# Kernel optimization log

Hardware: AMD Instinct MI355X
Metric: run time of the kernel (lower is better)

The kernel has to match this reference:

```python
import jax, jax.numpy as jnp
import numpy as np

B, T, D = 2, 2048, 1024
H, DK, DV = 16, 64, 64
DFF = 4096
EPS = 1e-6


def layer_norm(x, gamma, beta):
    # Matches the torch module: unbiased std (ddof=1), eps added to std,
    # gamma multiplied before dividing by (std + eps).
    mean = x.mean(axis=-1, keepdims=True)
    std = x.std(axis=-1, ddof=1, keepdims=True)
    return (x - mean) * gamma / (std + EPS) + beta


def setup_inputs() -> dict:
    key = jax.random.key(0)
    ks = jax.random.split(key, 8)
    s = 0.02
    return {
        "x": jax.random.normal(ks[0], (B, T, D), dtype=jnp.float32),
        "w_q": jax.random.normal(ks[1], (D, H * DK), dtype=jnp.float32) * s,
        "w_k": jax.random.normal(ks[2], (D, H * DK), dtype=jnp.float32) * s,
        "w_v": jax.random.normal(ks[3], (D, H * DV), dtype=jnp.float32) * s,
        "w_o": jax.random.normal(ks[4], (H * DV, D), dtype=jnp.float32) * s,
        "b_o": jnp.zeros((D,), dtype=jnp.float32),
        "w_fc1": jax.random.normal(ks[5], (D, DFF), dtype=jnp.float32) * s,
        "b_fc1": jnp.zeros((DFF,), dtype=jnp.float32),
        "w_fc2": jax.random.normal(ks[6], (DFF, D), dtype=jnp.float32) * s,
        "b_fc2": jnp.zeros((D,), dtype=jnp.float32),
        "ln1_g": jnp.ones((D,), dtype=jnp.float32),
        "ln1_b": jnp.zeros((D,), dtype=jnp.float32),
        "ln2_g": jnp.ones((D,), dtype=jnp.float32),
        "ln2_b": jnp.zeros((D,), dtype=jnp.float32),
    }


def attention(h, w_q, w_k, w_v, w_o, b_o):
    b, t, _ = h.shape
    q = (h @ w_q).reshape(b, t, H, DK).transpose(0, 2, 1, 3)  # [b,h,t,dk]
    k = (h @ w_k).reshape(b, t, H, DK).transpose(0, 2, 1, 3)
    v = (h @ w_v).reshape(b, t, H, DV).transpose(0, 2, 1, 3)
    scores = jnp.einsum('bhqk,bhmk->bhqm', q, k)              # [b,h,t,t]
    causal = jnp.triu(jnp.ones((t, t), dtype=bool), k=1)
    scores = jnp.where(causal, -jnp.inf, scores)
    attn = jax.nn.softmax(scores / jnp.sqrt(jnp.float32(DK)), axis=-1)
    ctx = jnp.einsum('bhqm,bhmv->bhqv', attn, v)              # [b,h,t,dv]
    ctx = ctx.transpose(0, 2, 1, 3).reshape(b, t, H * DV)
    return ctx @ w_o + b_o


def reference(x, w_q, w_k, w_v, w_o, b_o, w_fc1, b_fc1, w_fc2, b_fc2,
              ln1_g, ln1_b, ln2_g, ln2_b):
    x = x + attention(layer_norm(x, ln1_g, ln1_b), w_q, w_k, w_v, w_o, b_o)
    h = layer_norm(x, ln2_g, ln2_b)
    mlp = jax.nn.gelu(h @ w_fc1 + b_fc1, approximate=False) @ w_fc2 + b_fc2
    return x + mlp
```

## Files before the change

### kernel.cpp

```cpp
#include <hip/hip_runtime.h>
#include <hip/hip_bf16.h>
#include <cstdint>

#define Bz 2
#define Tz 2048
#define Dz 1024
#define Hz 16
#define NR (Bz*Tz)

typedef __bf16 bf16;
typedef __bf16 bf16x8 __attribute__((ext_vector_type(8)));
typedef __bf16 bf16x4 __attribute__((ext_vector_type(4)));
typedef short  s16x4  __attribute__((ext_vector_type(4)));
typedef float  f32x4  __attribute__((ext_vector_type(4)));

typedef unsigned int u32as1 __attribute__((address_space(1)));
typedef unsigned int u32as3 __attribute__((address_space(3)));

__device__ __forceinline__ void gl2lds16(const void* gp, void* lp) {
    __builtin_amdgcn_global_load_lds((u32as1*)gp, (u32as3*)lp, 16, 0, 0);
}

__global__ void k_transpose_cvt(const float* __restrict__ W, bf16* __restrict__ WT,
                                int K, int N, float scale) {
    __shared__ float tile[32][33];
    const int n0 = blockIdx.x * 32, k0 = blockIdx.y * 32;
    const int tx = threadIdx.x, ty = threadIdx.y;
#pragma unroll
    for (int i = 0; i < 4; i++)
        tile[ty + i*8][tx] = W[(size_t)(k0 + ty + i*8) * N + n0 + tx];
    __syncthreads();
#pragma unroll
    for (int i = 0; i < 4; i++)
        WT[(size_t)(n0 + ty + i*8) * K + k0 + tx] = (bf16)(tile[tx][ty + i*8] * scale);
}

__global__ void k_vtrans(const bf16* __restrict__ qkv, bf16* __restrict__ Vt) {
    __shared__ bf16 tile[64][72];
    const int t0 = blockIdx.x * 64;
    const int bh = blockIdx.y;
    const int b = bh >> 4, h = bh & 15;
    const int tid = threadIdx.x;
    const int tr = tid >> 3, c8 = (tid & 7) * 8;
    const bf16* src = qkv + (size_t)b * Tz * 3072 + 2048 + h * 64;
#pragma unroll
    for (int i = 0; i < 2; i++) {
        bf16x8 v = *(const bf16x8*)(src + (size_t)(t0 + i*32 + tr) * 3072 + c8);
        *(bf16x8*)&tile[i*32 + tr][c8] = v;
    }
    __syncthreads();
    bf16* dst = Vt + (size_t)bh * 64 * Tz + t0;
#pragma unroll
    for (int i = 0; i < 2; i++) {
        const int vr = i*32 + tr;
        bf16x8 o;
#pragma unroll
        for (int j = 0; j < 8; j++) o[j] = tile[c8 + j][vr];
        *(bf16x8*)(dst + (size_t)vr * Tz + c8) = o;
    }
}

__global__ void k_layernorm(const float* __restrict__ X, const float* __restrict__ gam,
                            const float* __restrict__ bet, bf16* __restrict__ out) {
    const int row = blockIdx.x, t = threadIdx.x;
    const float4 v = ((const float4*)(X + (size_t)row * Dz))[t];
    float s  = v.x + v.y + v.z + v.w;
    float ss = v.x*v.x + v.y*v.y + v.z*v.z + v.w*v.w;
#pragma unroll
    for (int o = 1; o < 64; o <<= 1) { s += __shfl_xor(s, o); ss += __shfl_xor(ss, o); }
    __shared__ float rs[4], rss[4];
    if ((t & 63) == 0) { rs[t >> 6] = s; rss[t >> 6] = ss; }
    __syncthreads();
    s  = rs[0] + rs[1] + rs[2] + rs[3];
    ss = rss[0] + rss[1] + rss[2] + rss[3];
    const float mean = s * (1.f / Dz);
    const float var  = fmaxf((ss - s * mean) * (1.f / (Dz - 1)), 0.f);
    const float inv  = 1.f / (sqrtf(var) + 1e-6f);
    const float4 gv = ((const float4*)gam)[t];
    const float4 bv = ((const float4*)bet)[t];
    bf16x4 o;
    o[0] = (bf16)((v.x - mean) * gv.x * inv + bv.x);
    o[1] = (bf16)((v.y - mean) * gv.y * inv + bv.y);
    o[2] = (bf16)((v.z - mean) * gv.z * inv + bv.z);
    o[3] = (bf16)((v.w - mean) * gv.w * inv + bv.w);
    *(bf16x4*)(out + (size_t)row * Dz + t * 4) = o;
}

__global__ __launch_bounds__(256) void k_gemm(
    const bf16* __restrict__ A, const bf16* __restrict__ BT,
    int M, int N, int K,
    const float* __restrict__ bias, const float* __restrict__ resid,
    float* __restrict__ Cf, bf16* __restrict__ Cb, int act,
    float* __restrict__ Cpart, int nsplit)
{
    __shared__ bf16 lA[128 * 64];
    __shared__ bf16 lB[128 * 64];
    const int tid = threadIdx.x;
    const int w = tid >> 6, lane = tid & 63;
    const int q = lane >> 4, l16 = lane & 15;
    const int m0 = blockIdx.y * 128, n0 = blockIdx.x * 128;
    const int wm = (w >> 1) * 64, wn = (w & 1) * 64;

    const int srow = lane >> 3;
    const int skg  = (lane & 7) ^ srow;
    const bf16* Ab = A  + (size_t)(m0 + w * 32 + srow) * K + skg * 8;
    const bf16* Bb = BT + (size_t)(n0 + w * 32 + srow) * K + skg * 8;
    bf16* lAw = lA + w * 2048;
    bf16* lBw = lB + w * 2048;

    f32x4 acc[4][4] = {};

    const int kPer = K / nsplit;
    const int kBeg = blockIdx.z * kPer, kEnd = kBeg + kPer;
    for (int k0 = kBeg; k0 < kEnd; k0 += 64) {
#pragma unroll
        for (int i = 0; i < 4; i++) {
            gl2lds16(Ab + (size_t)i * 8 * K + k0, lAw + i * 512);
            gl2lds16(Bb + (size_t)i * 8 * K + k0, lBw + i * 512);
        }
        __syncthreads();
#pragma unroll
        for (int kh = 0; kh < 2; kh++) {
            const int sl = (((kh * 4 + q) ^ (l16 & 7)) * 8);
            bf16x8 af[4], bfr[4];
#pragma unroll
            for (int t = 0; t < 4; t++) {
                af[t]  = *(const bf16x8*)(lA + (wm + t * 16 + l16) * 64 + sl);
                bfr[t] = *(const bf16x8*)(lB + (wn + t * 16 + l16) * 64 + sl);
            }
#pragma unroll
            for (int i = 0; i < 4; i++)
#pragma unroll
                for (int j = 0; j < 4; j++)
                    acc[i][j] = __builtin_amdgcn_mfma_f32_16x16x32_bf16(
                        af[i], bfr[j], acc[i][j], 0, 0, 0);
        }
        __syncthreads();
    }

    if (nsplit > 1) {
        float* P = Cpart + (size_t)blockIdx.z * M * N;
#pragma unroll
        for (int i = 0; i < 4; i++) {
            const int gr = m0 + wm + i * 16 + q * 4;
#pragma unroll
            for (int j = 0; j < 4; j++) {
                const int gc = n0 + wn + j * 16 + l16;
#pragma unroll
                for (int r = 0; r < 4; r++)
                    P[(size_t)(gr + r) * N + gc] = acc[i][j][r];
            }
        }
        return;
    }

#pragma unroll
    for (int i = 0; i < 4; i++) {
        const int gr = m0 + wm + i * 16 + q * 4;
#pragma unroll
        for (int j = 0; j < 4; j++) {
            const int gc = n0 + wn + j * 16 + l16;
            const float bv = bias ? bias[gc] : 0.f;
#pragma unroll
            for (int r = 0; r < 4; r++) {
                float v = acc[i][j][r] + bv;
                if (act) v = 0.5f * v * (1.f + erff(v * 0.70710678118f));
                const size_t idx = (size_t)(gr + r) * N + gc;
                if (resid) v += resid[idx];
                if (Cf) Cf[idx] = v;
                else    Cb[idx] = (bf16)v;
            }
        }
    }
}

__global__ __launch_bounds__(256) void k_reduce(
    const float* __restrict__ part, int nsplit, size_t MN, int N,
    const float* __restrict__ bias, const float* __restrict__ resid,
    float* __restrict__ Cf, bf16* __restrict__ Cb, int act)
{
    const size_t i4 = ((size_t)blockIdx.x * 256 + threadIdx.x) * 4;
    float4 v = *(const float4*)(part + i4);
    for (int s = 1; s < nsplit; s++) {
        const float4 p = *(const float4*)(part + s * MN + i4);
        v.x += p.x; v.y += p.y; v.z += p.z; v.w += p.w;
    }
    const int col = (int)(i4 % N);
    if (bias) {
        const float4 bv = *(const float4*)(bias + col);
        v.x += bv.x; v.y += bv.y; v.z += bv.z; v.w += bv.w;
    }
    if (act) {
        v.x = 0.5f * v.x * (1.f + erff(v.x * 0.70710678118f));
        v.y = 0.5f * v.y * (1.f + erff(v.y * 0.70710678118f));
        v.z = 0.5f * v.z * (1.f + erff(v.z * 0.70710678118f));
        v.w = 0.5f * v.w * (1.f + erff(v.w * 0.70710678118f));
    }
    if (resid) {
        const float4 rv = *(const float4*)(resid + i4);
        v.x += rv.x; v.y += rv.y; v.z += rv.z; v.w += rv.w;
    }
    if (Cf) *(float4*)(Cf + i4) = v;
    else {
        bf16x4 o; o[0] = (bf16)v.x; o[1] = (bf16)v.y; o[2] = (bf16)v.z; o[3] = (bf16)v.w;
        *(bf16x4*)(Cb + i4) = o;
    }
}

__global__ __launch_bounds__(256) void k_attn(const bf16* __restrict__ qkv,
                                              const bf16* __restrict__ Vt,
                                              bf16* __restrict__ ctx)
{
    __shared__ __align__(16) char smem[34816];
    bf16* lK = (bf16*)smem;
    bf16* lV = (bf16*)(smem + 16384);
    f32x4* sAcc = (f32x4*)smem;
    float*  sM  = (float*)(smem + 32768);
    float*  sL  = (float*)(smem + 33792);

    const int tid = threadIdx.x, lane = tid & 63, w = tid >> 6;
    const int l16 = lane & 15, quad = lane >> 4;
    const int wq = w & 1, ws = w >> 1;
    const int pr = blockIdx.x;
    const int h = blockIdx.y, b = blockIdx.z;

    const bf16* Qp  = qkv + (size_t)b * Tz * 3072 + h * 64;
    const bf16* Kp  = Qp + 1024;
    const bf16* Vtp = Vt + (size_t)(b * Hz + h) * 64 * Tz;

    const int krow  = tid >> 3;
    const int kslot = (tid & 7) ^ (krow & 7);
    const bf16* Kg = Kp + (size_t)krow * 3072 + kslot * 8;
    const int vrow  = tid >> 4;
    const int vslot = (tid & 15) ^ (vrow & 7);
    const bf16* Vg = Vtp + (size_t)vrow * Tz + vslot * 8;

#pragma unroll
    for (int ti = 0; ti < 2; ti++) {
        const int t = ti ? (63 - pr) : pr;
        const int q0 = t * 32 + wq * 16;

        bf16x8 qf[2];
#pragma unroll
        for (int kh = 0; kh < 2; kh++)
            qf[kh] = *(const bf16x8*)(Qp + (size_t)(q0 + l16) * 3072 + kh*32 + quad*8);

        f32x4 acc[4] = {};
        float m = -1e30f, l = 0.f;

        const int keyEnd = t * 32 + 32;
        for (int ktB = 0; ktB < keyEnd; ktB += 128) {
            __syncthreads();
#pragma unroll
            for (int s = 0; s < 4; s++) {
                gl2lds16(Kg + (size_t)(ktB + s * 32) * 3072, lK + s * 2048 + w * 512);
                gl2lds16(Vg + (size_t)s * 16 * Tz + ktB,     lV + s * 2048 + w * 512);
            }
            __syncthreads();

            const int kt = ktB + ws * 64;
            if (kt <= q0 + 15) {
                f32x4 sv[4];
                const int sw = l16 & 7;
#pragma unroll
                for (int c = 0; c < 4; c++) {
                    const int R = ws * 64 + c * 16 + l16;
                    bf16x8 kf0 = *(const bf16x8*)(lK + R * 64 + ((quad     ^ sw) * 8));
                    bf16x8 kf1 = *(const bf16x8*)(lK + R * 64 + (((4+quad) ^ sw) * 8));
                    f32x4 z = {0.f, 0.f, 0.f, 0.f};
                    z = __builtin_amdgcn_mfma_f32_16x16x32_bf16(kf0, qf[0], z, 0, 0, 0);
                    z = __builtin_amdgcn_mfma_f32_16x16x32_bf16(kf1, qf[1], z, 0, 0, 0);
                    sv[c] = z;
                }
                if (kt + 63 > q0) {
#pragma unroll
                    for (int c = 0; c < 4; c++)
#pragma unroll
                        for (int r = 0; r < 4; r++)
                            if (kt + c*16 + quad*4 + r > q0 + l16) sv[c][r] = -1e30f;
                }
                float t0 = fmaxf(fmaxf(sv[0][0], sv[0][1]), fmaxf(sv[0][2], sv[0][3]));
                float t1 = fmaxf(fmaxf(sv[1][0], sv[1][1]), fmaxf(sv[1][2], sv[1][3]));
                float t2 = fmaxf(fmaxf(sv[2][0], sv[2][1]), fmaxf(sv[2][2], sv[2][3]));
                float t3 = fmaxf(fmaxf(sv[3][0], sv[3][1]), fmaxf(sv[3][2], sv[3][3]));
                float tm = fmaxf(fmaxf(t0, t1), fmaxf(t2, t3));
                tm = fmaxf(tm, __shfl_xor(tm, 16));
                tm = fmaxf(tm, __shfl_xor(tm, 32));
                if (__any(tm > m)) {
                    const float mn = fmaxf(m, tm);
                    const float a  = __expf(m - mn);
                    m = mn;
                    l *= a;
#pragma unroll
                    for (int vt = 0; vt < 4; vt++)
#pragma unroll
                        for (int r = 0; r < 4; r++) acc[vt][r] *= a;
                }
                float ts = 0.f;
#pragma unroll
                for (int c = 0; c < 4; c++) {
                    s16x4 vf[4];
                    const int gslot = ws * 8 + c * 2 + (quad >> 1);
#pragma unroll
                    for (int vt = 0; vt < 4; vt++) {
                        const int Rv = vt * 16 + l16;
                        vf[vt] = *(const s16x4*)(lV + Rv * 128 + ((gslot ^ (Rv & 7)) * 8)
                                                 + (quad & 1) * 4);
                    }
                    bf16x4 tb;
#pragma unroll
                    for (int r = 0; r < 4; r++) {
                        const float p = __expf(sv[c][r] - m);
                        ts += p;
                        tb[r] = (bf16)p;
                    }
                    const s16x4 pb = __builtin_bit_cast(s16x4, tb);
#pragma unroll
                    for (int vt = 0; vt < 4; vt++)
                        acc[vt] = __builtin_amdgcn_mfma_f32_16x16x16bf16_1k(
                            vf[vt], pb, acc[vt], 0, 0, 0);
                }
                ts += __shfl_xor(ts, 16);
                ts += __shfl_xor(ts, 32);
                l += ts;
            }
        }

        __syncthreads();
        if (ws == 1) {
            sM[wq * 64 + lane] = m;
            sL[wq * 64 + lane] = l;
#pragma unroll
            for (int vt = 0; vt < 4; vt++)
                sAcc[(wq * 4 + vt) * 64 + lane] = acc[vt];
        }
        __syncthreads();
        if (ws == 0) {
            const float m1 = sM[wq * 64 + lane], l1 = sL[wq * 64 + lane];
            const float M  = fmaxf(m, m1);
            const float a0 = __expf(m - M), a1 = __expf(m1 - M);
            const float inv = 1.f / (l * a0 + l1 * a1);
#pragma unroll
            for (int vt = 0; vt < 4; vt++) {
                const f32x4 o1 = sAcc[(wq * 4 + vt) * 64 + lane];
                bf16x4 o;
#pragma unroll
                for (int r = 0; r < 4; r++)
                    o[r] = (bf16)((acc[vt][r] * a0 + o1[r] * a1) * inv);
                *(bf16x4*)(ctx + (size_t)(b * Tz + q0 + l16) * 1024
                           + h * 64 + vt * 16 + quad * 4) = o;
            }
        }
    }
}

extern "C" void kernel_launch(void* const* d_in, const int* in_sizes, int n_in,
                              void* d_out, int out_size, void* d_ws, size_t ws_size,
                              hipStream_t stream)
{
    const float* x     = (const float*)d_in[0];
    const float* w_q   = (const float*)d_in[1];
    const float* w_k   = (const float*)d_in[2];
    const float* w_v   = (const float*)d_in[3];
    const float* w_o   = (const float*)d_in[4];
    const float* b_o   = (const float*)d_in[5];
    const float* w_fc1 = (const float*)d_in[6];
    const float* b_fc1 = (const float*)d_in[7];
    const float* w_fc2 = (const float*)d_in[8];
    const float* b_fc2 = (const float*)d_in[9];
    const float* ln1_g = (const float*)d_in[10];
    const float* ln1_b = (const float*)d_in[11];
    const float* ln2_g = (const float*)d_in[12];
    const float* ln2_b = (const float*)d_in[13];
    float* out = (float*)d_out;

    char* p = (char*)d_ws;
    bf16* wqkvT = (bf16*)p; p += (size_t)3072 * 1024 * 2;
    bf16* woT   = (bf16*)p; p += (size_t)1024 * 1024 * 2;
    bf16* wfc1T = (bf16*)p; p += (size_t)4096 * 1024 * 2;
    bf16* wfc2T = (bf16*)p; p += (size_t)1024 * 4096 * 2;
    bf16* h1    = (bf16*)p; p += (size_t)NR * 1024 * 2;
    bf16* qkv   = (bf16*)p; p += (size_t)NR * 3072 * 2;
    bf16* ctx   = (bf16*)p; p += (size_t)NR * 1024 * 2;
    float* y    = (float*)p; p += (size_t)NR * 1024 * 4;
    bf16* h2    = (bf16*)p; p += (size_t)NR * 1024 * 2;
    bf16* g     = (bf16*)p; p += (size_t)NR * 4096 * 2;
    bf16* Vt    = h1;
    float* projPart = (float*)g;
    float* fc2Part  = (float*)h1;

    const dim3 tb(32, 8);
    k_transpose_cvt<<<dim3(32, 32),  tb, 0, stream>>>(w_q,   wqkvT,             1024, 1024, 0.125f);
    k_transpose_cvt<<<dim3(32, 32),  tb, 0, stream>>>(w_k,   wqkvT + 1024*1024, 1024, 1024, 1.f);
    k_transpose_cvt<<<dim3(32, 32),  tb, 0, stream>>>(w_v,   wqkvT + 2048*1024, 1024, 1024, 1.f);
    k_transpose_cvt<<<dim3(32, 32),  tb, 0, stream>>>(w_o,   woT,               1024, 1024, 1.f);
    k_transpose_cvt<<<dim3(128, 32), tb, 0, stream>>>(w_fc1, wfc1T,             1024, 4096, 1.f);
    k_transpose_cvt<<<dim3(32, 128), tb, 0, stream>>>(w_fc2, wfc2T,             4096, 1024, 1.f);

    k_layernorm<<<NR, 256, 0, stream>>>(x, ln1_g, ln1_b, h1);
    k_gemm<<<dim3(3072/128, NR/128), 256, 0, stream>>>(h1, wqkvT, NR, 3072, 1024,
                                                       nullptr, nullptr, nullptr, qkv, 0,
                                                       nullptr, 1);
    k_vtrans<<<dim3(Tz/64, Bz*Hz), 256, 0, stream>>>(qkv, Vt);
    k_attn<<<dim3(32, Hz, Bz), 256, 0, stream>>>(qkv, Vt, ctx);

    k_gemm<<<dim3(1024/128, NR/128, 2), 256, 0, stream>>>(ctx, woT, NR, 1024, 1024,
                                                          nullptr, nullptr, nullptr, nullptr, 0,
                                                          projPart, 2);
    k_reduce<<<(size_t)NR * 1024 / 1024, 256, 0, stream>>>(projPart, 2, (size_t)NR * 1024, 1024,
                                                           b_o, x, y, nullptr, 0);

    k_layernorm<<<NR, 256, 0, stream>>>(y, ln2_g, ln2_b, h2);
    k_gemm<<<dim3(4096/128, NR/128), 256, 0, stream>>>(h2, wfc1T, NR, 4096, 1024,
                                                       b_fc1, nullptr, nullptr, g, 1,
                                                       nullptr, 1);
    k_gemm<<<dim3(1024/128, NR/128, 2), 256, 0, stream>>>(g, wfc2T, NR, 1024, 4096,
                                                          nullptr, nullptr, nullptr, nullptr, 0,
                                                          fc2Part, 2);
    k_reduce<<<(size_t)NR * 1024 / 1024, 256, 0, stream>>>(fc2Part, 2, (size_t)NR * 1024, 1024,
                                                           b_fc2, y, out, nullptr, 0);
    (void)in_sizes; (void)n_in; (void)out_size; (void)ws_size;
}
```

Measured before the change: 424.1 us.

## Fuse split-K reduce with LayerNorm, use bf16 partials and 4-way split

Split-K partial sums for the output projection and FC2 are now stored in bf16 instead of fp32, and the split factor is raised from 2 to 4 to create more workgroups. The projection's reduce kernel is fused with the second LayerNorm, removing one kernel launch and a full read of y. The aim is to cut partial-sum memory traffic and improve GPU fill, at the cost of lost precision in the partial sums and more partial data per element.

```diff
diff --git a/kernel.cpp b/kernel.cpp
--- a/kernel.cpp
+++ b/kernel.cpp
@@ -91,7 +91,7 @@
     int M, int N, int K,
     const float* __restrict__ bias, const float* __restrict__ resid,
     float* __restrict__ Cf, bf16* __restrict__ Cb, int act,
-    float* __restrict__ Cpart, int nsplit)
+    bf16* __restrict__ Pb, int nsplit)
 {
     __shared__ bf16 lA[128 * 64];
     __shared__ bf16 lB[128 * 64];
@@ -139,7 +139,7 @@
     }
 
     if (nsplit > 1) {
-        float* P = Cpart + (size_t)blockIdx.z * M * N;
+        bf16* P = Pb + (size_t)blockIdx.z * M * N;
 #pragma unroll
         for (int i = 0; i < 4; i++) {
             const int gr = m0 + wm + i * 16 + q * 4;
@@ -148,7 +148,7 @@
                 const int gc = n0 + wn + j * 16 + l16;
 #pragma unroll
                 for (int r = 0; r < 4; r++)
-                    P[(size_t)(gr + r) * N + gc] = acc[i][j][r];
+                    P[(size_t)(gr + r) * N + gc] = (bf16)acc[i][j][r];
             }
         }
         return;
@@ -174,37 +174,65 @@
     }
 }
 
-__global__ __launch_bounds__(256) void k_reduce(
-    const float* __restrict__ part, int nsplit, size_t MN, int N,
+__global__ __launch_bounds__(256) void k_reduce_ln(
+    const bf16* __restrict__ part, size_t MN,
     const float* __restrict__ bias, const float* __restrict__ resid,
-    float* __restrict__ Cf, bf16* __restrict__ Cb, int act)
+    float* __restrict__ y,
+    const float* __restrict__ gam, const float* __restrict__ bet,
+    bf16* __restrict__ h2)
+{
+    const int row = blockIdx.x, t = threadIdx.x;
+    const size_t i4 = (size_t)row * Dz + t * 4;
+    float4 v = {0.f, 0.f, 0.f, 0.f};
+#pragma unroll
+    for (int s = 0; s < 4; s++) {
+        const bf16x4 p = *(const bf16x4*)(part + s * MN + i4);
+        v.x += (float)p[0]; v.y += (float)p[1]; v.z += (float)p[2]; v.w += (float)p[3];
+    }
+    const float4 bv = ((const float4*)bias)[t];
+    const float4 rv = *(const float4*)(resid + i4);
+    v.x += bv.x + rv.x; v.y += bv.y + rv.y; v.z += bv.z + rv.z; v.w += bv.w + rv.w;
+    *(float4*)(y + i4) = v;
+
+    float s  = v.x + v.y + v.z + v.w;
+    float ss = v.x*v.x + v.y*v.y + v.z*v.z + v.w*v.w;
+#pragma unroll
+    for (int o = 1; o < 64; o <<= 1) { s += __shfl_xor(s, o); ss += __shfl_xor(ss, o); }
+    __shared__ float rs[4], rss[4];
+    if ((t & 63) == 0) { rs[t >> 6] = s; rss[t >> 6] = ss; }
+    __syncthreads();
+    s  = rs[0] + rs[1] + rs[2] + rs[3];
+    ss = rss[0] + rss[1] + rss[2] + rss[3];
+    const float mean = s * (1.f / Dz);
+    const float var  = fmaxf((ss - s * mean) * (1.f / (Dz - 1)), 0.f);
+    const float inv  = 1.f / (sqrtf(var) + 1e-6f);
+    const float4 gv = ((const float4*)gam)[t];
+    const float4 be = ((const float4*)bet)[t];
+    bf16x4 o;
+    o[0] = (bf16)((v.x - mean) * gv.x * inv + be.x);
+    o[1] = (bf16)((v.y - mean) * gv.y * inv + be.y);
+    o[2] = (bf16)((v.z - mean) * gv.z * inv + be.z);
+    o[3] = (bf16)((v.w - mean) * gv.w * inv + be.w);
+    *(bf16x4*)(h2 + i4) = o;
+}
+
+__global__ __launch_bounds__(256) void k_reduce_out(
+    const bf16* __restrict__ part, size_t MN, int N,
+    const float* __restrict__ bias, const float* __restrict__ resid,
+    float* __restrict__ out)
 {
     const size_t i4 = ((size_t)blockIdx.x * 256 + threadIdx.x) * 4;
-    float4 v = *(const float4*)(part + i4);
-    for (int s = 1; s < nsplit; s++) {
-        const float4 p = *(const float4*)(part + s * MN + i4);
-        v.x += p.x; v.y += p.y; v.z += p.z; v.w += p.w;
+    float4 v = {0.f, 0.f, 0.f, 0.f};
+#pragma unroll
+    for (int s = 0; s < 4; s++) {
+        const bf16x4 p = *(const bf16x4*)(part + s * MN + i4);
+        v.x += (float)p[0]; v.y += (float)p[1]; v.z += (float)p[2]; v.w += (float)p[3];
     }
     const int col = (int)(i4 % N);
-    if (bias) {
-        const float4 bv = *(const float4*)(bias + col);
-        v.x += bv.x; v.y += bv.y; v.z += bv.z; v.w += bv.w;
-    }
-    if (act) {
-        v.x = 0.5f * v.x * (1.f + erff(v.x * 0.70710678118f));
-        v.y = 0.5f * v.y * (1.f + erff(v.y * 0.70710678118f));
-        v.z = 0.5f * v.z * (1.f + erff(v.z * 0.70710678118f));
-        v.w = 0.5f * v.w * (1.f + erff(v.w * 0.70710678118f));
-    }
-    if (resid) {
-        const float4 rv = *(const float4*)(resid + i4);
-        v.x += rv.x; v.y += rv.y; v.z += rv.z; v.w += rv.w;
-    }
-    if (Cf) *(float4*)(Cf + i4) = v;
-    else {
-        bf16x4 o; o[0] = (bf16)v.x; o[1] = (bf16)v.y; o[2] = (bf16)v.z; o[3] = (bf16)v.w;
-        *(bf16x4*)(Cb + i4) = o;
-    }
+    const float4 bv = *(const float4*)(bias + col);
+    const float4 rv = *(const float4*)(resid + i4);
+    v.x += bv.x + rv.x; v.y += bv.y + rv.y; v.z += bv.z + rv.z; v.w += bv.w + rv.w;
+    *(float4*)(out + i4) = v;
 }
 
 __global__ __launch_bounds__(256) void k_attn(const bf16* __restrict__ qkv,
@@ -386,8 +414,9 @@
     bf16* h2    = (bf16*)p; p += (size_t)NR * 1024 * 2;
     bf16* g     = (bf16*)p; p += (size_t)NR * 4096 * 2;
     bf16* Vt    = h1;
-    float* projPart = (float*)g;
-    float* fc2Part  = (float*)h1;
+    bf16* projPart = g;
+    bf16* fc2Part  = h1;
+    const size_t MN = (size_t)NR * 1024;
 
     const dim3 tb(32, 8);
     k_transpose_cvt<<<dim3(32, 32),  tb, 0, stream>>>(w_q,   wqkvT,             1024, 1024, 0.125f);
@@ -404,20 +433,17 @@
     k_vtrans<<<dim3(Tz/64, Bz*Hz), 256, 0, stream>>>(qkv, Vt);
     k_attn<<<dim3(32, Hz, Bz), 256, 0, stream>>>(qkv, Vt, ctx);
 
-    k_gemm<<<dim3(1024/128, NR/128, 2), 256, 0, stream>>>(ctx, woT, NR, 1024, 1024,
+    k_gemm<<<dim3(1024/128, NR/128, 4), 256, 0, stream>>>(ctx, woT, NR, 1024, 1024,
                                                           nullptr, nullptr, nullptr, nullptr, 0,
-                                                          projPart, 2);
-    k_reduce<<<(size_t)NR * 1024 / 1024, 256, 0, stream>>>(projPart, 2, (size_t)NR * 1024, 1024,
-                                                           b_o, x, y, nullptr, 0);
-
-    k_layernorm<<<NR, 256, 0, stream>>>(y, ln2_g, ln2_b, h2);
+                                                          projPart, 4);
+    k_reduce_ln<<<NR, 256, 0, stream>>>(projPart, MN, b_o, x, y, ln2_g, ln2_b, h2);
+
     k_gemm<<<dim3(4096/128, NR/128), 256, 0, stream>>>(h2, wfc1T, NR, 4096, 1024,
                                                        b_fc1, nullptr, nullptr, g, 1,
                                                        nullptr, 1);
-    k_gemm<<<dim3(1024/128, NR/128, 2), 256, 0, stream>>>(g, wfc2T, NR, 1024, 4096,
+    k_gemm<<<dim3(1024/128, NR/128, 4), 256, 0, stream>>>(g, wfc2T, NR, 1024, 4096,
                                                           nullptr, nullptr, nullptr, nullptr, 0,
-                                                          fc2Part, 2);
-    k_reduce<<<(size_t)NR * 1024 / 1024, 256, 0, stream>>>(fc2Part, 2, (size_t)NR * 1024, 1024,
-                                                           b_fc2, y, out, nullptr, 0);
+                                                          fc2Part, 4);
+    k_reduce_out<<<MN / 1024, 256, 0, stream>>>(fc2Part, MN, 1024, b_fc2, y, out);
     (void)in_sizes; (void)n_in; (void)out_size; (void)ws_size;
 }
```

Result: no change. 426.0 us (+0.5%).
